# Kernel tuning notes

Hardware: AMD Instinct MI355X
Metric: run time of the kernel (lower is better)

## Reference

```python
import jax, jax.numpy as jnp
import numpy as np

EPS = 1e-5

def _bn_relu(y, mean, var, scale, bias):
    # y: (b, c, n); eval-mode batchnorm over channel axis, then ReLU
    inv = scale / jnp.sqrt(var + EPS)
    return jax.nn.relu((y - mean[None, :, None]) * inv[None, :, None] + bias[None, :, None])

def setup_inputs() -> dict:
    key = jax.random.key(0)
    ks = jax.random.split(key, 6)
    b, c, n, cr = 4, 256, 4096, 32
    inp = {
        'x': jax.random.normal(ks[0], (b, c, n), jnp.float32),
        'w_q': jax.random.normal(ks[1], (cr, c), jnp.float32) * (1.0 / np.sqrt(c)),
        'w_k': jax.random.normal(ks[2], (cr, c), jnp.float32) * (1.0 / np.sqrt(c)),
        'w_v': jax.random.normal(ks[3], (c, c), jnp.float32) * (1.0 / np.sqrt(c)),
        'bn1_scale': jnp.ones((cr,), jnp.float32), 'bn1_bias': jnp.zeros((cr,), jnp.float32),
        'bn1_mean': jnp.zeros((cr,), jnp.float32), 'bn1_var': jnp.ones((cr,), jnp.float32),
        'bn2_scale': jnp.ones((cr,), jnp.float32), 'bn2_bias': jnp.zeros((cr,), jnp.float32),
        'bn2_mean': jnp.zeros((cr,), jnp.float32), 'bn2_var': jnp.ones((cr,), jnp.float32),
        'bn3_scale': jnp.ones((c,), jnp.float32), 'bn3_bias': jnp.zeros((c,), jnp.float32),
        'bn3_mean': jnp.zeros((c,), jnp.float32), 'bn3_var': jnp.ones((c,), jnp.float32),
        'gamma': jax.random.normal(ks[4], (1,), jnp.float32),
    }
    return inp

def reference(x, w_q, w_k, w_v,
              bn1_scale, bn1_bias, bn1_mean, bn1_var,
              bn2_scale, bn2_bias, bn2_mean, bn2_var,
              bn3_scale, bn3_bias, bn3_mean, bn3_var,
              gamma):
    # x: (b, c, n). Original views as (b, c, n, 1) so width=1, height=n.
    b, c, n = x.shape
    # 1x1 conv == channel matmul, then BN+ReLU
    q = _bn_relu(jnp.einsum('oc,bcn->bon', w_q, x), bn1_mean, bn1_var, bn1_scale, bn1_bias)  # (b, c', n)
    k = _bn_relu(jnp.einsum('oc,bcn->bon', w_k, x), bn2_mean, bn2_var, bn2_scale, bn2_bias)  # (b, c', n)
    v = _bn_relu(jnp.einsum('oc,bcn->bon', w_v, x), bn3_mean, bn3_var, bn3_scale, bn3_bias)  # (b, c, n)
    # energy_H: (b, n, n) with -inf diagonal (self-attention along 'height')
    energy_h = jnp.einsum('bdi,bdj->bij', q, k)
    eye = jnp.eye(n, dtype=bool)
    energy_h = jnp.where(eye[None], -jnp.inf, energy_h)
    # energy_W: width=1 -> per-position self energy (b, n)
    energy_w = jnp.sum(q * k, axis=1)
    # softmax over concat of n H-logits and 1 W-logit
    att = jax.nn.softmax(jnp.concatenate([energy_h, energy_w[..., None]], axis=-1), axis=-1)  # (b, n, n+1)
    att_h = att[..., :n]        # (b, n, n), query i -> key j
    att_w = att[..., n]         # (b, n)
    out_h = jnp.einsum('bcj,bij->bci', v, att_h)   # aggregate values along height
    out_w = v * att_w[:, None, :]                  # width=1 self term
    out = gamma[0] * (out_h + out_w) + x
    return out
```

## Files before the change

kernel.cpp:

```cpp
#include <hip/hip_runtime.h>

#define Bb 4
#define Cc 256
#define Nn 4096
#define CR 32
#define EPS_BN 1e-5f
#define SHIFT2 28.853900817779268f
#define LOG2E  1.4426950408889634f
#define JSPLIT 2
#define JSL (Nn / JSPLIT)
#define TJ 128
#define NTILES (JSL / TJ)

typedef __attribute__((ext_vector_type(8))) short short8;
typedef __attribute__((ext_vector_type(4))) float f32x4;

__device__ inline unsigned int pk2(float a, float b) {
    __bf16 ha = (__bf16)a, hb = (__bf16)b;
    unsigned short ra = __builtin_bit_cast(unsigned short, ha);
    unsigned short rb = __builtin_bit_cast(unsigned short, hb);
    return ((unsigned int)rb << 16) | ra;
}
__device__ inline float blo(unsigned int u) { return __uint_as_float(u << 16); }
__device__ inline float bhi(unsigned int u) { return __uint_as_float(u & 0xffff0000u); }
__device__ inline float ex2(float x) { return __builtin_amdgcn_exp2f(x); }

__global__ __launch_bounds__(256) void prep_w(
    const float* __restrict__ wq, const float* __restrict__ wk,
    const float* __restrict__ wv, __bf16* __restrict__ Wf)
{
    const int r16 = blockIdx.x;
    const int tid = threadIdx.x;
#pragma unroll
    for (int ss = 0; ss < 2; ++ss) {
        int s = tid + ss * 256;
        int kc = s >> 6, lane = s & 63;
        int R = r16 * 16 + (lane & 15);
        const float* src = (R < 32) ? (wq + (size_t)R * Cc)
                         : (R < 64) ? (wk + (size_t)(R - 32) * Cc)
                                    : (wv + (size_t)(R - 64) * Cc);
        const float* p = src + kc * 32 + (lane >> 4) * 8;
        float4 a = *(const float4*)p;
        float4 c2 = *(const float4*)(p + 4);
        uint4 pk = { pk2(a.x,a.y), pk2(a.z,a.w), pk2(c2.x,c2.y), pk2(c2.z,c2.w) };
        *(uint4*)&Wf[(((size_t)r16 * 8 + kc) * 64 + lane) * 8] = pk;
    }
}

__global__ __launch_bounds__(256) void qkv_kernel(
    const float* __restrict__ x, const __bf16* __restrict__ Wf,
    const float* __restrict__ bn1s, const float* __restrict__ bn1b, const float* __restrict__ bn1m, const float* __restrict__ bn1v,
    const float* __restrict__ bn2s, const float* __restrict__ bn2b, const float* __restrict__ bn2m, const float* __restrict__ bn2v,
    const float* __restrict__ bn3s, const float* __restrict__ bn3b, const float* __restrict__ bn3m, const float* __restrict__ bn3v,
    __bf16* __restrict__ Qt, __bf16* __restrict__ Kt, __bf16* __restrict__ Vb)
{
    __shared__ __align__(16) float  sXf[4][32 * 40];
    __shared__ __align__(16) __bf16 sXt[4][2][32 * 40];
    __shared__ __align__(16) __bf16 oT[128 * 136];

    const int tid = threadIdx.x;
    const int n0 = blockIdx.x * 128, g = blockIdx.y, b = blockIdx.z;
    const int lane = tid & 63, w = tid >> 6;
    const int l15 = lane & 15, l4 = lane >> 4;
    const int nmt = (g == 0) ? 4 : 8;
    const int r16b = (g == 0) ? 0 : 4 + (g - 1) * 8;

    float*  sXfw  = &sXf[w][0];
    __bf16* sXtw0 = &sXt[w][0][0];
    __bf16* sXtw1 = &sXt[w][1][0];

    const int cr = lane >> 3, nq = lane & 7;
    const float* xbase = x + (size_t)(b * Cc + cr) * Nn + n0 + w * 32 + nq * 4;

    float4 xg[4];
#pragma unroll
    for (int it = 0; it < 4; ++it)
        xg[it] = *(const float4*)&xbase[(size_t)(it * 8) * Nn];

    f32x4 acc[8][2];
#pragma unroll
    for (int mt = 0; mt < 8; ++mt)
#pragma unroll
        for (int nt = 0; nt < 2; ++nt) acc[mt][nt] = (f32x4){0.f, 0.f, 0.f, 0.f};

    for (int kc = 0; kc < 8; ++kc) {
#pragma unroll
        for (int it = 0; it < 4; ++it)
            *(float4*)&sXfw[(it * 8 + cr) * 40 + nq * 4] = xg[it];

        if (kc + 1 < 8) {
#pragma unroll
            for (int it = 0; it < 4; ++it)
                xg[it] = *(const float4*)&xbase[(size_t)((kc + 1) * 32 + it * 8) * Nn];
        }

#pragma unroll
        for (int s = 0; s < 2; ++s) {
            int n = lane & 31, c0 = (lane >> 5) * 8 + s * 16;
            float h[8], lo[8];
#pragma unroll
            for (int j = 0; j < 8; ++j) {
                float v = sXfw[(c0 + j) * 40 + n];
                float hh = (float)(__bf16)v;
                h[j] = hh; lo[j] = v - hh;
            }
            uint4 H = { pk2(h[0],h[1]), pk2(h[2],h[3]), pk2(h[4],h[5]), pk2(h[6],h[7]) };
            uint4 L = { pk2(lo[0],lo[1]), pk2(lo[2],lo[3]), pk2(lo[4],lo[5]), pk2(lo[6],lo[7]) };
            *(uint4*)&sXtw0[n * 40 + c0] = H;
            *(uint4*)&sXtw1[n * 40 + c0] = L;
        }

        short8 bh[2], bl[2];
#pragma unroll
        for (int nt = 0; nt < 2; ++nt) {
            bh[nt] = *(const short8*)&sXtw0[(nt * 16 + l15) * 40 + l4 * 8];
            bl[nt] = *(const short8*)&sXtw1[(nt * 16 + l15) * 40 + l4 * 8];
        }
        short8 af[8];
#pragma unroll
        for (int mt = 0; mt < 8; ++mt)
            if (mt < nmt)
                af[mt] = *(const short8*)&Wf[(((size_t)(r16b + mt) * 8 + kc) * 64 + lane) * 8];
#pragma unroll
        for (int mt = 0; mt < 8; ++mt) {
            if (mt < nmt) {
#pragma unroll
                for (int nt = 0; nt < 2; ++nt) {
                    acc[mt][nt] = __builtin_amdgcn_mfma_f32_16x16x32_bf16(af[mt], bh[nt], acc[mt][nt], 0, 0, 0);
                    acc[mt][nt] = __builtin_amdgcn_mfma_f32_16x16x32_bf16(af[mt], bl[nt], acc[mt][nt], 0, 0, 0);
                }
            }
        }
    }

    if (g == 0) {
#pragma unroll
        for (int mt = 0; mt < 4; ++mt) {
            float scl[4], off[4];
#pragma unroll
            for (int r = 0; r < 4; ++r) {
                int R = mt * 16 + l4 * 4 + r;
                float s, o;
                if (R < 32) {
                    s = bn1s[R] * __frsqrt_rn(bn1v[R] + EPS_BN);
                    o = bn1b[R] - bn1m[R] * s;
                } else {
                    int row = R - 32;
                    s = bn2s[row] * __frsqrt_rn(bn2v[row] + EPS_BN);
                    o = bn2b[row] - bn2m[row] * s;
                    s *= LOG2E; o *= LOG2E;
                }
                scl[r] = s; off[r] = o;
            }
            __bf16* dst = (mt < 2) ? Qt : Kt;
            int d0 = (mt & 1) * 16 + l4 * 4;
#pragma unroll
            for (int nt = 0; nt < 2; ++nt) {
                f32x4 a = acc[mt][nt];
                float e0 = fmaxf(fmaf(a.x, scl[0], off[0]), 0.f);
                float e1 = fmaxf(fmaf(a.y, scl[1], off[1]), 0.f);
                float e2 = fmaxf(fmaf(a.z, scl[2], off[2]), 0.f);
                float e3 = fmaxf(fmaf(a.w, scl[3], off[3]), 0.f);
                uint2 p = { pk2(e0, e1), pk2(e2, e3) };
                int n = n0 + w * 32 + nt * 16 + l15;
                *(uint2*)&dst[(size_t)(b * Nn + n) * CR + d0] = p;
            }
        }
    } else {
        const int vr0 = (g - 1) * 128;
#pragma unroll
        for (int mt = 0; mt < 8; ++mt) {
            float scl[4], off[4];
#pragma unroll
            for (int r = 0; r < 4; ++r) {
                int row = vr0 + mt * 16 + l4 * 4 + r;
                float s = bn3s[row] * __frsqrt_rn(bn3v[row] + EPS_BN);
                scl[r] = s; off[r] = bn3b[row] - bn3m[row] * s;
            }
#pragma unroll
            for (int nt = 0; nt < 2; ++nt) {
                f32x4 a = acc[mt][nt];
                float e[4];
                e[0] = fmaxf(fmaf(a.x, scl[0], off[0]), 0.f);
                e[1] = fmaxf(fmaf(a.y, scl[1], off[1]), 0.f);
                e[2] = fmaxf(fmaf(a.z, scl[2], off[2]), 0.f);
                e[3] = fmaxf(fmaf(a.w, scl[3], off[3]), 0.f);
                int ncol = w * 32 + nt * 16 + l15;
#pragma unroll
                for (int r = 0; r < 4; ++r)
                    oT[(mt * 16 + l4 * 4 + r) * 136 + ncol] = (__bf16)e[r];
            }
        }
        __syncthreads();
        int rr = tid >> 1, qq = tid & 1;
        size_t vrow = (size_t)(b * Cc + vr0 + rr) * Nn + n0 + qq * 64;
#pragma unroll
        for (int e8 = 0; e8 < 8; ++e8)
            *(uint4*)&Vb[vrow + e8 * 8] = *(const uint4*)&oT[rr * 136 + qq * 64 + e8 * 8];
    }
}

__global__ __launch_bounds__(512) void attn_kernel(
    const __bf16* __restrict__ Qt, const __bf16* __restrict__ Kt,
    const __bf16* __restrict__ Vb,
    __bf16* __restrict__ PO, float* __restrict__ PL)
{
    __shared__ __align__(16) __bf16 sQ[64 * 40];
    __shared__ __align__(16) __bf16 sP[64 * 128];
    __shared__ __align__(16) float  sL[8][64];

    const int tid = threadIdx.x, lane = tid & 63, w = tid >> 6;
    const int b = blockIdx.z, js = blockIdx.y, iblk = blockIdx.x;
    const int i0 = iblk * 64;
    const int l15 = lane & 15, l4 = lane >> 4;

    if (tid < 256) {
        int i = tid >> 2, o = tid & 3;
        *(uint4*)&sQ[i * 40 + o * 8] =
            *(const uint4*)&Qt[(size_t)(b * Nn + i0 + i) * CR + o * 8];
    }
    __syncthreads();

    short8 qf[4];
#pragma unroll
    for (int it = 0; it < 4; ++it)
        qf[it] = *(const short8*)&sQ[(it * 16 + l15) * 40 + l4 * 8];

    f32x4 oacc[8];
#pragma unroll
    for (int z = 0; z < 8; ++z) oacc[z] = (f32x4){0.f, 0.f, 0.f, 0.f};
    float lp[4] = {0.f, 0.f, 0.f, 0.f};

    const size_t jb = (size_t)js * JSL;
    short8 kf = *(const short8*)&Kt[(size_t)(b * Nn + jb + 16 * w + l15) * CR + l4 * 8];
    const __bf16* vrow0 = Vb + (size_t)(b * Cc + w * 32 + l15) * Nn;

    char* sPb = (char*)sP;
    const int wcolw = w * 32 + l4 * 8;

    for (int t = 0; t < NTILES; ++t) {
        const size_t j0 = jb + (size_t)t * TJ;

        short8 v0[2], v1[2];
#pragma unroll
        for (int ct = 0; ct < 2; ++ct)
            v0[ct] = *(const short8*)&vrow0[(size_t)(ct * 16) * Nn + j0 + l4 * 8];
#pragma unroll
        for (int ct = 0; ct < 2; ++ct)
            v1[ct] = *(const short8*)&vrow0[(size_t)(ct * 16) * Nn + j0 + 32 + l4 * 8];

#pragma unroll
        for (int it = 0; it < 4; ++it) {
            f32x4 c0 = (f32x4){0.f, 0.f, 0.f, 0.f};
            c0 = __builtin_amdgcn_mfma_f32_16x16x32_bf16(kf, qf[it], c0, 0, 0, 0);
            float e0 = ex2(c0.x - SHIFT2);
            float e1 = ex2(c0.y - SHIFT2);
            float e2 = ex2(c0.z - SHIFT2);
            float e3 = ex2(c0.w - SHIFT2);
            lp[it] += (e0 + e1) + (e2 + e3);
            uint2 p2 = { pk2(e0, e1), pk2(e2, e3) };
            int row = it * 16 + l15;
            *(uint2*)(sPb + row * 256 + (wcolw ^ ((row & 7) << 4))) = p2;
        }
        __syncthreads();

        if (t + 1 < NTILES)
            kf = *(const short8*)&Kt[(size_t)(b * Nn + j0 + TJ + 16 * w + l15) * CR + l4 * 8];

        __builtin_amdgcn_s_setprio(1);
        {
            short8 pf[4];
#pragma unroll
            for (int it = 0; it < 4; ++it) {
                int row = it * 16 + l15;
                pf[it] = *(const short8*)(sPb + row * 256 + ((l4 * 16) ^ ((row & 7) << 4)));
            }
#pragma unroll
            for (int ct = 0; ct < 2; ++ct)
#pragma unroll
                for (int it = 0; it < 4; ++it)
                    oacc[it * 2 + ct] = __builtin_amdgcn_mfma_f32_16x16x32_bf16(
                        pf[it], v0[ct], oacc[it * 2 + ct], 0, 0, 0);
        }
#pragma unroll
        for (int ct = 0; ct < 2; ++ct)
            v0[ct] = *(const short8*)&vrow0[(size_t)(ct * 16) * Nn + j0 + 64 + l4 * 8];
        {
            short8 pf[4];
#pragma unroll
            for (int it = 0; it < 4; ++it) {
                int row = it * 16 + l15;
                pf[it] = *(const short8*)(sPb + row * 256 + ((64 + l4 * 16) ^ ((row & 7) << 4)));
            }
#pragma unroll
            for (int ct = 0; ct < 2; ++ct)
#pragma unroll
                for (int it = 0; it < 4; ++it)
                    oacc[it * 2 + ct] = __builtin_amdgcn_mfma_f32_16x16x32_bf16(
                        pf[it], v1[ct], oacc[it * 2 + ct], 0, 0, 0);
        }
#pragma unroll
        for (int ct = 0; ct < 2; ++ct)
            v1[ct] = *(const short8*)&vrow0[(size_t)(ct * 16) * Nn + j0 + 96 + l4 * 8];
        {
            short8 pf[4];
#pragma unroll
            for (int it = 0; it < 4; ++it) {
                int row = it * 16 + l15;
                pf[it] = *(const short8*)(sPb + row * 256 + ((128 + l4 * 16) ^ ((row & 7) << 4)));
            }
#pragma unroll
            for (int ct = 0; ct < 2; ++ct)
#pragma unroll
                for (int it = 0; it < 4; ++it)
                    oacc[it * 2 + ct] = __builtin_amdgcn_mfma_f32_16x16x32_bf16(
                        pf[it], v0[ct], oacc[it * 2 + ct], 0, 0, 0);
        }
        {
            short8 pf[4];
#pragma unroll
            for (int it = 0; it < 4; ++it) {
                int row = it * 16 + l15;
                pf[it] = *(const short8*)(sPb + row * 256 + ((192 + l4 * 16) ^ ((row & 7) << 4)));
            }
#pragma unroll
            for (int ct = 0; ct < 2; ++ct)
#pragma unroll
                for (int it = 0; it < 4; ++it)
                    oacc[it * 2 + ct] = __builtin_amdgcn_mfma_f32_16x16x32_bf16(
                        pf[it], v1[ct], oacc[it * 2 + ct], 0, 0, 0);
        }
        __builtin_amdgcn_s_setprio(0);
        __syncthreads();
    }

#pragma unroll
    for (int it = 0; it < 4; ++it) {
        float v = lp[it];
        v += __shfl_xor(v, 16);
        v += __shfl_xor(v, 32);
        if (lane < 16) sL[w][it * 16 + lane] = v;
    }
    __syncthreads();
    if (tid < 64) {
        float s = 0.f;
#pragma unroll
        for (int w8 = 0; w8 < 8; ++w8) s += sL[w8][tid];
        PL[(size_t)(js * Bb + b) * Nn + i0 + tid] = s;
    }

    const size_t base = (size_t)((js * Bb + b) * (Nn / 64) + iblk) * 16384;
#pragma unroll
    for (int it = 0; it < 4; ++it)
#pragma unroll
        for (int ct = 0; ct < 2; ++ct) {
            f32x4 a = oacc[it * 2 + ct];
            uint2 p = { pk2(a.x, a.y), pk2(a.z, a.w) };
            int g16 = w * 2 + ct;
            int s = (g16 >> 2) * 16 + it * 4 + (g16 & 3);
            *(uint2*)&PO[base + (size_t)(s * 64 + lane) * 4] = p;
        }
}

__global__ __launch_bounds__(256) void reduce_kernel(
    const __bf16* __restrict__ PO, const float* __restrict__ PL,
    const float* __restrict__ x, const float* __restrict__ gamma,
    float* __restrict__ out)
{
    __shared__ __align__(16) float oT[64 * 68];
    __shared__ float sLinv[64];

    const int tid = threadIdx.x;
    const int iblk = blockIdx.x, wq = blockIdx.y, b = blockIdx.z;
    const int i0 = iblk * 64;
    const int lane = tid & 63, ct = tid >> 6, l15 = lane & 15, l4 = lane >> 4;

    if (tid < 64) {
        float l = 0.f;
#pragma unroll
        for (int js = 0; js < JSPLIT; ++js)
            l += PL[(size_t)(js * Bb + b) * Nn + i0 + tid];
        sLinv[tid] = 1.0f / l;
    }

    float o[4][4];
#pragma unroll
    for (int it = 0; it < 4; ++it) {
        o[it][0] = o[it][1] = o[it][2] = o[it][3] = 0.f;
#pragma unroll
        for (int js = 0; js < JSPLIT; ++js) {
            size_t base = (size_t)((js * Bb + b) * (Nn / 64) + iblk) * 16384;
            uint2 v = *(const uint2*)&PO[base + (size_t)((((wq * 4 + it) * 4 + ct) * 64 + lane)) * 4];
            o[it][0] += blo(v.x); o[it][1] += bhi(v.x);
            o[it][2] += blo(v.y); o[it][3] += bhi(v.y);
        }
    }

    const int cl = ct * 16 + l15;
#pragma unroll
    for (int it = 0; it < 4; ++it) {
        float4 t4 = { o[it][0], o[it][1], o[it][2], o[it][3] };
        *(float4*)&oT[cl * 68 + it * 16 + l4 * 4] = t4;
    }
    __syncthreads();

    const float g = gamma[0];
    const int c_l = tid >> 2, icol = (tid & 3) * 16;
    const int cg = wq * 64 + c_l;
    const size_t gb = (size_t)(b * Cc + cg) * Nn + i0 + icol;
#pragma unroll
    for (int k4 = 0; k4 < 4; ++k4) {
        float4 ov = *(const float4*)&oT[c_l * 68 + icol + k4 * 4];
        float4 li = *(const float4*)&sLinv[icol + k4 * 4];
        float4 xv = *(const float4*)&x[gb + k4 * 4];
        float4 res;
        res.x = fmaf(g, ov.x * li.x, xv.x);
        res.y = fmaf(g, ov.y * li.y, xv.y);
        res.z = fmaf(g, ov.z * li.z, xv.z);
        res.w = fmaf(g, ov.w * li.w, xv.w);
        *(float4*)&out[gb + k4 * 4] = res;
    }
}

extern "C" void kernel_launch(void* const* d_in, const int* in_sizes, int n_in,
                              void* d_out, int out_size, void* d_ws, size_t ws_size,
                              hipStream_t stream)
{
    const float* x    = (const float*)d_in[0];
    const float* wq   = (const float*)d_in[1];
    const float* wk   = (const float*)d_in[2];
    const float* wv   = (const float*)d_in[3];
    const float* bn1s = (const float*)d_in[4];
    const float* bn1b = (const float*)d_in[5];
    const float* bn1m = (const float*)d_in[6];
    const float* bn1v = (const float*)d_in[7];
    const float* bn2s = (const float*)d_in[8];
    const float* bn2b = (const float*)d_in[9];
    const float* bn2m = (const float*)d_in[10];
    const float* bn2v = (const float*)d_in[11];
    const float* bn3s = (const float*)d_in[12];
    const float* bn3b = (const float*)d_in[13];
    const float* bn3m = (const float*)d_in[14];
    const float* bn3v = (const float*)d_in[15];
    const float* gmm  = (const float*)d_in[16];
    float* out = (float*)d_out;

    char* ws = (char*)d_ws;
    __bf16* Qt  = (__bf16*)(ws);
    __bf16* Kt  = (__bf16*)(ws + (1u << 20));
    __bf16* Vb  = (__bf16*)(ws + (2u << 20));
    char*   big = ws + (10u << 20);
    __bf16* PO  = (__bf16*)big;
    float*  PL  = (float*)(big + 33554432);
    __bf16* Wf  = (__bf16*)(big + 33554432 + 262144);

    prep_w<<<dim3(20), 256, 0, stream>>>(wq, wk, wv, Wf);

    qkv_kernel<<<dim3(Nn / 128, 3, Bb), 256, 0, stream>>>(
        x, Wf,
        bn1s, bn1b, bn1m, bn1v,
        bn2s, bn2b, bn2m, bn2v,
        bn3s, bn3b, bn3m, bn3v,
        Qt, Kt, Vb);

    attn_kernel<<<dim3(Nn / 64, JSPLIT, Bb), 512, 0, stream>>>(Qt, Kt, Vb, PO, PL);

    reduce_kernel<<<dim3(Nn / 64, 4, Bb), 256, 0, stream>>>(PO, PL, x, gmm, out);
}
```

Measured before the change: 203.3 us.

## Precompute transposed bf16 hi/lo split of x in a separate kernel

Adds a split_x kernel that transposes x to (b, n, c) and splits each value into bf16 high and low parts once. qkv_kernel then loads MFMA B fragments straight from global memory instead of staging, transposing and splitting x in LDS for each of its three channel groups. The intent is to stop repeating the conversion three times and to drop the LDS traffic and register pressure inside the matmul loop. The cost is an extra launch plus a write and reread of 16 MB of bf16 intermediates. The workspace is also repacked to fit the new buffers.

```diff
diff --git a/kernel.cpp b/kernel.cpp
--- a/kernel.cpp
+++ b/kernel.cpp
@@ -47,15 +47,54 @@
     }
 }
 
+__global__ __launch_bounds__(256) void split_x(
+    const float* __restrict__ x,
+    __bf16* __restrict__ xhi, __bf16* __restrict__ xlo)
+{
+    __shared__ __align__(16) float tile[64][68];
+    const int tid = threadIdx.x;
+    const int n0 = blockIdx.x * 64, c0 = blockIdx.y * 64, b = blockIdx.z;
+
+    {
+        int r = tid >> 2, q = tid & 3;
+        const float* src = &x[(size_t)(b * Cc + c0 + r) * Nn + n0 + q * 16];
+#pragma unroll
+        for (int u = 0; u < 4; ++u)
+            *(float4*)&tile[r][q * 16 + u * 4] = *(const float4*)&src[u * 4];
+    }
+    __syncthreads();
+
+    {
+        int nr = tid >> 2, oc = tid & 3;
+        uint4 H[2], L[2];
+#pragma unroll
+        for (int u = 0; u < 2; ++u) {
+            float h[8], lo8[8];
+#pragma unroll
+            for (int j = 0; j < 8; ++j) {
+                float v = tile[oc * 16 + u * 8 + j][nr];
+                float hh = (float)(__bf16)v;
+                h[j] = hh; lo8[j] = v - hh;
+            }
+            H[u] = (uint4){ pk2(h[0],h[1]), pk2(h[2],h[3]), pk2(h[4],h[5]), pk2(h[6],h[7]) };
+            L[u] = (uint4){ pk2(lo8[0],lo8[1]), pk2(lo8[2],lo8[3]), pk2(lo8[4],lo8[5]), pk2(lo8[6],lo8[7]) };
+        }
+        size_t base = (size_t)(b * Nn + n0 + nr) * Cc + c0 + oc * 16;
+        *(uint4*)&xhi[base]     = H[0];
+        *(uint4*)&xhi[base + 8] = H[1];
+        *(uint4*)&xlo[base]     = L[0];
+        *(uint4*)&xlo[base + 8] = L[1];
+    }
+}
+
 __global__ __launch_bounds__(256) void qkv_kernel(
-    const float* __restrict__ x, const __bf16* __restrict__ Wf,
+    const __bf16* __restrict__ xhi, const __bf16* __restrict__ xlo,
+    const __bf16* __restrict__ Wf,
     const float* __restrict__ bn1s, const float* __restrict__ bn1b, const float* __restrict__ bn1m, const float* __restrict__ bn1v,
     const float* __restrict__ bn2s, const float* __restrict__ bn2b, const float* __restrict__ bn2m, const float* __restrict__ bn2v,
     const float* __restrict__ bn3s, const float* __restrict__ bn3b, const float* __restrict__ bn3m, const float* __restrict__ bn3v,
     __bf16* __restrict__ Qt, __bf16* __restrict__ Kt, __bf16* __restrict__ Vb)
 {
-    __shared__ __align__(16) float  sXf[4][32 * 40];
-    __shared__ __align__(16) __bf16 sXt[4][2][32 * 40];
     __shared__ __align__(16) __bf16 oT[128 * 136];
 
     const int tid = threadIdx.x;
@@ -65,17 +104,9 @@
     const int nmt = (g == 0) ? 4 : 8;
     const int r16b = (g == 0) ? 0 : 4 + (g - 1) * 8;
 
-    float*  sXfw  = &sXf[w][0];
-    __bf16* sXtw0 = &sXt[w][0][0];
-    __bf16* sXtw1 = &sXt[w][1][0];
-
-    const int cr = lane >> 3, nq = lane & 7;
-    const float* xbase = x + (size_t)(b * Cc + cr) * Nn + n0 + w * 32 + nq * 4;
-
-    float4 xg[4];
-#pragma unroll
-    for (int it = 0; it < 4; ++it)
-        xg[it] = *(const float4*)&xbase[(size_t)(it * 8) * Nn];
+    const size_t bfoff = (size_t)(b * Nn + n0 + w * 32 + l15) * Cc + l4 * 8;
+    const __bf16* bh0 = xhi + bfoff;
+    const __bf16* bl0 = xlo + bfoff;
 
     f32x4 acc[8][2];
 #pragma unroll
@@ -84,50 +115,20 @@
         for (int nt = 0; nt < 2; ++nt) acc[mt][nt] = (f32x4){0.f, 0.f, 0.f, 0.f};
 
     for (int kc = 0; kc < 8; ++kc) {
-#pragma unroll
-        for (int it = 0; it < 4; ++it)
-            *(float4*)&sXfw[(it * 8 + cr) * 40 + nq * 4] = xg[it];
-
-        if (kc + 1 < 8) {
-#pragma unroll
-            for (int it = 0; it < 4; ++it)
-                xg[it] = *(const float4*)&xbase[(size_t)((kc + 1) * 32 + it * 8) * Nn];
-        }
-
-#pragma unroll
-        for (int s = 0; s < 2; ++s) {
-            int n = lane & 31, c0 = (lane >> 5) * 8 + s * 16;
-            float h[8], lo[8];
-#pragma unroll
-            for (int j = 0; j < 8; ++j) {
-                float v = sXfw[(c0 + j) * 40 + n];
-                float hh = (float)(__bf16)v;
-                h[j] = hh; lo[j] = v - hh;
-            }
-            uint4 H = { pk2(h[0],h[1]), pk2(h[2],h[3]), pk2(h[4],h[5]), pk2(h[6],h[7]) };
-            uint4 L = { pk2(lo[0],lo[1]), pk2(lo[2],lo[3]), pk2(lo[4],lo[5]), pk2(lo[6],lo[7]) };
-            *(uint4*)&sXtw0[n * 40 + c0] = H;
-            *(uint4*)&sXtw1[n * 40 + c0] = L;
-        }
-
         short8 bh[2], bl[2];
 #pragma unroll
         for (int nt = 0; nt < 2; ++nt) {
-            bh[nt] = *(const short8*)&sXtw0[(nt * 16 + l15) * 40 + l4 * 8];
-            bl[nt] = *(const short8*)&sXtw1[(nt * 16 + l15) * 40 + l4 * 8];
-        }
-        short8 af[8];
-#pragma unroll
-        for (int mt = 0; mt < 8; ++mt)
-            if (mt < nmt)
-                af[mt] = *(const short8*)&Wf[(((size_t)(r16b + mt) * 8 + kc) * 64 + lane) * 8];
+            bh[nt] = *(const short8*)&bh0[(size_t)(nt * 16) * Cc + kc * 32];
+            bl[nt] = *(const short8*)&bl0[(size_t)(nt * 16) * Cc + kc * 32];
+        }
 #pragma unroll
         for (int mt = 0; mt < 8; ++mt) {
             if (mt < nmt) {
+                short8 af = *(const short8*)&Wf[(((size_t)(r16b + mt) * 8 + kc) * 64 + lane) * 8];
 #pragma unroll
                 for (int nt = 0; nt < 2; ++nt) {
-                    acc[mt][nt] = __builtin_amdgcn_mfma_f32_16x16x32_bf16(af[mt], bh[nt], acc[mt][nt], 0, 0, 0);
-                    acc[mt][nt] = __builtin_amdgcn_mfma_f32_16x16x32_bf16(af[mt], bl[nt], acc[mt][nt], 0, 0, 0);
+                    acc[mt][nt] = __builtin_amdgcn_mfma_f32_16x16x32_bf16(af, bh[nt], acc[mt][nt], 0, 0, 0);
+                    acc[mt][nt] = __builtin_amdgcn_mfma_f32_16x16x32_bf16(af, bl[nt], acc[mt][nt], 0, 0, 0);
                 }
             }
         }
@@ -449,15 +450,18 @@
     __bf16* Qt  = (__bf16*)(ws);
     __bf16* Kt  = (__bf16*)(ws + (1u << 20));
     __bf16* Vb  = (__bf16*)(ws + (2u << 20));
-    char*   big = ws + (10u << 20);
-    __bf16* PO  = (__bf16*)big;
-    float*  PL  = (float*)(big + 33554432);
-    __bf16* Wf  = (__bf16*)(big + 33554432 + 262144);
+    __bf16* PO  = (__bf16*)(ws + (10u << 20));
+    float*  PL  = (float*)(ws + (26u << 20));
+    __bf16* Wf  = (__bf16*)(ws + (26u << 20) + 262144);
+    __bf16* xhi = (__bf16*)(ws + (27u << 20));
+    __bf16* xlo = (__bf16*)(ws + (35u << 20));
 
     prep_w<<<dim3(20), 256, 0, stream>>>(wq, wk, wv, Wf);
 
+    split_x<<<dim3(Nn / 64, Cc / 64, Bb), 256, 0, stream>>>(x, xhi, xlo);
+
     qkv_kernel<<<dim3(Nn / 128, 3, Bb), 256, 0, stream>>>(
-        x, Wf,
+        xhi, xlo, Wf,
         bn1s, bn1b, bn1m, bn1v,
         bn2s, bn2b, bn2m, bn2v,
         bn3s, bn3b, bn3m, bn3v,
```

Result: no change. 203.0 us (-0.1%).
